# Performance work log

Measured on AMD Instinct MI355X. Metric: run time of the kernel, lower is better.

## Reference

```python
import jax, jax.numpy as jnp
import numpy as np

B, S, D = 2, 2048, 4096
N_HEADS, N_KV_HEADS, HEAD_DIM = 32, 8, 128
Q_DIM = N_HEADS * HEAD_DIM        # 4096
KV_DIM = N_KV_HEADS * HEAD_DIM    # 1024
N_REP = N_HEADS // N_KV_HEADS
ROPE_THETA = 500000.0


def make_freqs_cis(seqlen, head_dim, theta):
    # Interleaved (sin, cos) pairs per rotary frequency, matching the module's
    # einsum/flip RoPE convention: row1 = x0*sin + x1*cos, row0 = x0*cos - x1*sin.
    inv_freq = 1.0 / (theta ** (np.arange(0, head_dim, 2, dtype=np.float32) / head_dim))
    t = np.arange(seqlen, dtype=np.float32)
    ang = np.outer(t, inv_freq)                       # [S, hd/2]
    fc = np.stack([np.sin(ang), np.cos(ang)], axis=-1)  # [S, hd/2, 2]
    return jnp.asarray(fc.reshape(seqlen, head_dim))


def apply_rotary_emb(xq, xk, freqs_cis):
    # xq: [B,S,Hq,hd], xk: [B,S,Hkv,hd], freqs_cis: [S,hd]
    xq_shape, xk_shape = xq.shape, xk.shape
    xq2 = xq.reshape(*xq.shape[:-1], -1, 2)
    xk2 = xk.reshape(*xk.shape[:-1], -1, 2)
    fc = freqs_cis.reshape(freqs_cis.shape[0], 1, -1, 2)   # [S,1,hd/2,2]
    # row_1 = <x, fc>
    xq_row1 = jnp.einsum('bshpi,shpi->bshp', xq2, fc)
    xk_row1 = jnp.einsum('bshpi,shpi->bshp', xk2, fc)
    # flipped fc with negated second component: (f1, -f0)
    fc_flip = jnp.flip(fc, axis=-1) * jnp.array([1.0, -1.0], dtype=fc.dtype)
    xq_row0 = jnp.einsum('bshpi,shpi->bshp', xq2, fc_flip)
    xk_row0 = jnp.einsum('bshpi,shpi->bshp', xk2, fc_flip)
    xq_out = jnp.stack([xq_row0, xq_row1], axis=-1).reshape(xq_shape)
    xk_out = jnp.stack([xk_row0, xk_row1], axis=-1).reshape(xk_shape)
    return xq_out, xk_out


def setup_inputs() -> dict:
    key = jax.random.key(0)
    k1, k2, k3 = jax.random.split(key, 3)
    x = jax.random.normal(k1, (B, S, D), dtype=jnp.float32)
    wqkv = jax.random.normal(k2, (D, Q_DIM + 2 * KV_DIM), dtype=jnp.float32) * 0.02
    wo = jax.random.normal(k3, (Q_DIM, D), dtype=jnp.float32) * 0.02
    freqs_cis = make_freqs_cis(S, HEAD_DIM, ROPE_THETA)
    return {"x": x, "freqs_cis": freqs_cis, "wqkv": wqkv, "wo": wo, "is_causal": 1}


def reference(x, freqs_cis, wqkv, wo, is_causal):
    bsz, seqlen, _ = x.shape
    xqkv = jnp.einsum('bsd,de->bse', x, wqkv)
    xq = xqkv[..., :Q_DIM].reshape(bsz, seqlen, N_HEADS, HEAD_DIM)
    xk = xqkv[..., Q_DIM:Q_DIM + KV_DIM].reshape(bsz, seqlen, N_KV_HEADS, HEAD_DIM)
    xv = xqkv[..., Q_DIM + KV_DIM:].reshape(bsz, seqlen, N_KV_HEADS, HEAD_DIM)
    xq, xk = apply_rotary_emb(xq, xk, freqs_cis)
    # [B,H,S,hd]
    xq = xq.transpose(0, 2, 1, 3)
    xk = jnp.repeat(xk.transpose(0, 2, 1, 3), N_REP, axis=1)
    xv = jnp.repeat(xv.transpose(0, 2, 1, 3), N_REP, axis=1)
    scale = 1.0 / jnp.sqrt(jnp.asarray(HEAD_DIM, dtype=xq.dtype))
    scores = jnp.einsum('bhqd,bhkd->bhqk', xq, xk) * scale
    if is_causal:
        mask = jnp.tril(jnp.ones((seqlen, seqlen), dtype=bool))
        scores = jnp.where(mask, scores, jnp.finfo(scores.dtype).min)
    attn = jax.nn.softmax(scores, axis=-1)
    out = jnp.einsum('bhqk,bhkd->bhqd', attn, xv)
    out = out.transpose(0, 2, 1, 3).reshape(bsz, seqlen, Q_DIM)
    return jnp.einsum('bsd,de->bse', out, wo)
```

## Files before the change

### kernel.cpp

```cpp
#include <hip/hip_runtime.h>
#include <stdint.h>
#include <stddef.h>

#define BB 2
#define SS 2048
#define DD 4096
#define NH 32
#define NKV 8
#define HD 128
#define QDIM 4096
#define KVDIM 1024
#define NQKV 6144
#define NTILES 64
#define QK_SCALE_L2E 0.12751744f

typedef __bf16 bf16;
typedef __bf16 bf16x8 __attribute__((ext_vector_type(8)));
typedef __bf16 bf16x4 __attribute__((ext_vector_type(4)));
typedef float f32x4 __attribute__((ext_vector_type(4)));

#define MFMA16(a, b, c) __builtin_amdgcn_mfma_f32_16x16x32_bf16((a), (b), (c), 0, 0, 0)
#define BAR() __builtin_amdgcn_s_barrier()
#define VMW10() asm volatile("s_waitcnt vmcnt(10)" ::: "memory")
#define VMW8() asm volatile("s_waitcnt vmcnt(8)" ::: "memory")
#define VMW7() asm volatile("s_waitcnt vmcnt(7)" ::: "memory")

typedef __attribute__((address_space(1))) void GASV;
typedef __attribute__((address_space(3))) void LASV;

__device__ __forceinline__ void gload_lds16(const void* g, void* l) {
    __builtin_amdgcn_global_load_lds((GASV*)g, (LASV*)l, 16, 0, 0);
}

__device__ __forceinline__ float fexp2(float x) {
    float r;
    asm("v_exp_f32 %0, %1" : "=v"(r) : "v"(x));
    return r;
}

__global__ __launch_bounds__(256) void k_cvt_x(const float* __restrict__ in,
                                               bf16* __restrict__ out) {
    size_t i = ((size_t)blockIdx.x * 256 + threadIdx.x) * 8;
    const float4 a = *(const float4*)(in + i);
    const float4 b = *(const float4*)(in + i + 4);
    bf16x8 v;
    v[0] = (bf16)a.x; v[1] = (bf16)a.y; v[2] = (bf16)a.z; v[3] = (bf16)a.w;
    v[4] = (bf16)b.x; v[5] = (bf16)b.y; v[6] = (bf16)b.z; v[7] = (bf16)b.w;
    *(bf16x8*)(out + i) = v;
}

__global__ __launch_bounds__(256) void k_tr_cvt(const float* __restrict__ in,
                                                bf16* __restrict__ out, int R, int C) {
    __shared__ float tile[64][65];
    const int t = threadIdx.x;
    const int tx = t & 15, ty = t >> 4;
    const int r0 = blockIdx.y * 64, c0 = blockIdx.x * 64;
#pragma unroll
    for (int p = 0; p < 4; ++p) {
        const float4 v = *(const float4*)(in + (size_t)(r0 + p * 16 + ty) * C + c0 + tx * 4);
        tile[p * 16 + ty][tx * 4 + 0] = v.x;
        tile[p * 16 + ty][tx * 4 + 1] = v.y;
        tile[p * 16 + ty][tx * 4 + 2] = v.z;
        tile[p * 16 + ty][tx * 4 + 3] = v.w;
    }
    __syncthreads();
#pragma unroll
    for (int p = 0; p < 4; ++p) {
        const int oc = c0 + p * 16 + ty;
        bf16x4 pk;
#pragma unroll
        for (int j = 0; j < 4; ++j) pk[j] = (bf16)tile[tx * 4 + j][p * 16 + ty];
        *(bf16x4*)(out + (size_t)oc * R + r0 + tx * 4) = pk;
    }
}

__device__ __forceinline__ void stage_half(char* ldsRegion, const bf16* gsrc) {
    const int t = threadIdx.x;
    const int wid = t >> 6;
#pragma unroll
    for (int i = 0; i < 2; ++i) {
        const int off = i * 8192 + t * 16;
        const int row = off >> 7;
        const int pc = (off >> 4) & 7;
        const int lc = pc ^ (row & 7);
        gload_lds16(gsrc + (size_t)row * 4096 + lc * 8,
                    ldsRegion + i * 8192 + wid * 1024);
    }
}

__device__ __forceinline__ void gemm256(const bf16* __restrict__ At,
                                        const bf16* __restrict__ Bt,
                                        char* LB, f32x4 acc[8][4]) {
    const int tid = threadIdx.x, lane = tid & 63, wid = tid >> 6;
    const int wm = wid >> 2, wn = wid & 3;
    const int l15 = lane & 15, l4 = lane >> 4;

    const f32x4 vz = {0.f, 0.f, 0.f, 0.f};
#pragma unroll
    for (int m = 0; m < 8; ++m)
#pragma unroll
        for (int n = 0; n < 4; ++n) acc[m][n] = vz;

    auto Areg = [&](int db, int h) -> char* { return LB + db * 32768 + h * 16384; };
    auto Breg = [&](int db, int h) -> char* { return LB + 65536 + db * 32768 + h * 16384; };

    bf16x8 RA[2][4], RAb[2][4], RB0[2][2], RB1[2][2];

    auto loadA = [&](bf16x8 dst[2][4], int db, int h) {
        char* base = Areg(db, h);
#pragma unroll
        for (int kk = 0; kk < 2; ++kk)
#pragma unroll
            for (int mf = 0; mf < 4; ++mf) {
                const int row = wm * 64 + mf * 16 + l15;
                const int cc = kk * 4 + l4;
                dst[kk][mf] = *(const bf16x8*)(base + row * 128 + ((cc ^ (row & 7)) << 4));
            }
    };
    auto loadB = [&](bf16x8 dst[2][2], int db, int h) {
        char* base = Breg(db, h);
#pragma unroll
        for (int kk = 0; kk < 2; ++kk)
#pragma unroll
            for (int nf = 0; nf < 2; ++nf) {
                const int row = wn * 32 + nf * 16 + l15;
                const int cc = kk * 4 + l4;
                dst[kk][nf] = *(const bf16x8*)(base + row * 128 + ((cc ^ (row & 7)) << 4));
            }
    };
    auto stA = [&](int tau, int h) {
        stage_half(Areg(tau & 1, h), At + (size_t)(h * 128) * 4096 + tau * 64);
    };
    auto stB = [&](int tau, int h) {
        stage_half(Breg(tau & 1, h), Bt + (size_t)(h * 128) * 4096 + tau * 64);
    };
    auto mma = [&](bf16x8 A[2][4], bf16x8 B[2][2], int mb, int nb) {
        __builtin_amdgcn_s_setprio(1);
#pragma unroll
        for (int kk = 0; kk < 2; ++kk)
#pragma unroll
            for (int mf = 0; mf < 4; ++mf)
#pragma unroll
                for (int nf = 0; nf < 2; ++nf)
                    acc[mb + mf][nb + nf] = MFMA16(A[kk][mf], B[kk][nf], acc[mb + mf][nb + nf]);
        __builtin_amdgcn_s_setprio(0);
    };

    stA(0, 0); stB(0, 0); stB(0, 1); stA(0, 1);
    stA(1, 0); stB(1, 0); stB(1, 1); stA(1, 1);
    VMW8();
    BAR();
    loadA(RA, 0, 0); loadB(RB0, 0, 0);

#pragma unroll 1
    for (int tau = 0; tau < NTILES - 2; ++tau) {
        const int db = tau & 1, ndb = db ^ 1;
        loadB(RB1, db, 1);
        stA(tau + 2, 0);
        BAR();
        mma(RA, RB0, 0, 0);
        BAR();
        loadA(RAb, db, 1);
        stB(tau + 2, 0);
        BAR();
        mma(RA, RB1, 0, 2);
        BAR();
        stB(tau + 2, 1);
        VMW10();
        BAR();
        mma(RAb, RB0, 4, 0);
        BAR();
        loadA(RA, ndb, 0);
        loadB(RB0, ndb, 0);
        stA(tau + 2, 1);
        VMW8();
        BAR();
        mma(RAb, RB1, 4, 2);
        BAR();
    }

    asm volatile("s_waitcnt vmcnt(0)" ::: "memory");
    BAR();
#pragma unroll 1
    for (int tau = NTILES - 2; tau < NTILES; ++tau) {
        const int db = tau & 1, ndb = db ^ 1;
        loadB(RB1, db, 1);
        mma(RA, RB0, 0, 0);
        loadA(RAb, db, 1);
        mma(RA, RB1, 0, 2);
        mma(RAb, RB0, 4, 0);
        if (tau < NTILES - 1) { loadA(RA, ndb, 0); loadB(RB0, ndb, 0); }
        mma(RAb, RB1, 4, 2);
    }
}

__device__ __forceinline__ void stage_B192(char* ldsRegion, const bf16* gsrc) {
    const int t = threadIdx.x;
    const int wid = t >> 6;
#pragma unroll
    for (int i = 0; i < 3; ++i) {
        const int off = i * 8192 + t * 16;
        const int row = off >> 7;
        const int pc = (off >> 4) & 7;
        const int lc = pc ^ (row & 7);
        gload_lds16(gsrc + (size_t)row * 4096 + lc * 8,
                    ldsRegion + i * 8192 + wid * 1024);
    }
}

__device__ __forceinline__ void gemm192(const bf16* __restrict__ At,
                                        const bf16* __restrict__ Bt,
                                        char* LB, f32x4 acc[8][3]) {
    const int tid = threadIdx.x, lane = tid & 63, wid = tid >> 6;
    const int wm = wid >> 2, wn = wid & 3;
    const int l15 = lane & 15, l4 = lane >> 4;

    const f32x4 vz = {0.f, 0.f, 0.f, 0.f};
#pragma unroll
    for (int m = 0; m < 8; ++m)
#pragma unroll
        for (int n = 0; n < 3; ++n) acc[m][n] = vz;

    auto Areg = [&](int db, int h) -> char* { return LB + db * 32768 + h * 16384; };
    auto Breg = [&](int db) -> char* { return LB + 65536 + db * 24576; };

    bf16x8 RA[2][4], RAb[2][4], RB0[2][2], RB1[2];

    auto loadA = [&](bf16x8 dst[2][4], int db, int h) {
        char* base = Areg(db, h);
#pragma unroll
        for (int kk = 0; kk < 2; ++kk)
#pragma unroll
            for (int mf = 0; mf < 4; ++mf) {
                const int row = wm * 64 + mf * 16 + l15;
                const int cc = kk * 4 + l4;
                dst[kk][mf] = *(const bf16x8*)(base + row * 128 + ((cc ^ (row & 7)) << 4));
            }
    };
    auto loadB0 = [&](int db) {
        char* base = Breg(db);
#pragma unroll
        for (int kk = 0; kk < 2; ++kk)
#pragma unroll
            for (int nf = 0; nf < 2; ++nf) {
                const int row = wn * 48 + nf * 16 + l15;
                const int cc = kk * 4 + l4;
                RB0[kk][nf] = *(const bf16x8*)(base + row * 128 + ((cc ^ (row & 7)) << 4));
            }
    };
    auto loadB1 = [&](int db) {
        char* base = Breg(db);
#pragma unroll
        for (int kk = 0; kk < 2; ++kk) {
            const int row = wn * 48 + 32 + l15;
            const int cc = kk * 4 + l4;
            RB1[kk] = *(const bf16x8*)(base + row * 128 + ((cc ^ (row & 7)) << 4));
        }
    };
    auto stA = [&](int tau, int h) {
        stage_half(Areg(tau & 1, h), At + (size_t)(h * 128) * 4096 + tau * 64);
    };
    auto stB = [&](int tau) {
        stage_B192(Breg(tau & 1), Bt + tau * 64);
    };
    auto mmaB0 = [&](bf16x8 A[2][4], int mb) {
        __builtin_amdgcn_s_setprio(1);
#pragma unroll
        for (int kk = 0; kk < 2; ++kk)
#pragma unroll
            for (int mf = 0; mf < 4; ++mf)
#pragma unroll
                for (int nf = 0; nf < 2; ++nf)
                    acc[mb + mf][nf] = MFMA16(A[kk][mf], RB0[kk][nf], acc[mb + mf][nf]);
        __builtin_amdgcn_s_setprio(0);
    };
    auto mmaB1 = [&](bf16x8 A[2][4], int mb) {
        __builtin_amdgcn_s_setprio(1);
#pragma unroll
        for (int kk = 0; kk < 2; ++kk)
#pragma unroll
            for (int mf = 0; mf < 4; ++mf)
                acc[mb + mf][2] = MFMA16(A[kk][mf], RB1[kk], acc[mb + mf][2]);
        __builtin_amdgcn_s_setprio(0);
    };

    stA(0, 0); stB(0); stA(0, 1);
    stA(1, 0); stB(1); stA(1, 1);
    VMW7();
    BAR();
    loadA(RA, 0, 0); loadB0(0);

#pragma unroll 1
    for (int tau = 0; tau < NTILES - 2; ++tau) {
        const int db = tau & 1, ndb = db ^ 1;
        loadB1(db);
        stA(tau + 2, 0);
        BAR();
        mmaB0(RA, 0);
        BAR();
        loadA(RAb, db, 1);
        stB(tau + 2);
        BAR();
        mmaB1(RA, 0);
        BAR();
        stA(tau + 2, 1);
        VMW7();
        BAR();
        mmaB0(RAb, 4);
        BAR();
        loadA(RA, ndb, 0);
        loadB0(ndb);
        BAR();
        mmaB1(RAb, 4);
        BAR();
    }

    asm volatile("s_waitcnt vmcnt(0)" ::: "memory");
    BAR();
#pragma unroll 1
    for (int tau = NTILES - 2; tau < NTILES; ++tau) {
        const int db = tau & 1, ndb = db ^ 1;
        loadB1(db);
        mmaB0(RA, 0);
        loadA(RAb, db, 1);
        mmaB1(RA, 0);
        mmaB0(RAb, 4);
        if (tau < NTILES - 1) { loadA(RA, ndb, 0); loadB0(ndb); }
        mmaB1(RAb, 4);
    }
}

__device__ __forceinline__ void xcd_swizzle(int gx, int& bx, int& by) {
    const int nwg = gx * gridDim.y;
    int lin = by * gx + bx;
    lin = (lin & 7) * (nwg >> 3) + (lin >> 3);
    bx = lin % gx;
    by = lin / gx;
}

__global__ __launch_bounds__(512, 2) void k_gemm_qkv(const bf16* __restrict__ A,
                                                     const bf16* __restrict__ Bt,
                                                     const float* __restrict__ fc,
                                                     bf16* __restrict__ Qb,
                                                     bf16* __restrict__ Kb,
                                                     bf16* __restrict__ VTb) {
    __shared__ __align__(16) char LB[114688];
    f32x4 acc[8][3];
    int bx = blockIdx.x, by = blockIdx.y;
    xcd_swizzle(NQKV / 192, bx, by);
    gemm192(A + (size_t)by * 256 * 4096, Bt + (size_t)bx * 192 * 4096, LB, acc);

    const int tid = threadIdx.x, lane = tid & 63, wid = tid >> 6;
    const int wm = wid >> 2, wn = wid & 3;
    const int l15 = lane & 15, l4 = lane >> 4;
#pragma unroll
    for (int mf = 0; mf < 8; ++mf) {
        const int rowbase = by * 256 + (mf >> 2) * 128 + wm * 64 + (mf & 3) * 16 + l4 * 4;
#pragma unroll
        for (int nf = 0; nf < 3; ++nf) {
            const int rb = bx * 192 + wn * 48 + nf * 16;
            const int col = rb + l15;
            f32x4 v = acc[mf][nf];
            if (rb < QDIM + KVDIM) {
                const int d = col & (HD - 1);
                const int dp = d & ~1;
                const float sgn = (d & 1) ? 1.f : -1.f;
#pragma unroll
                for (int r = 0; r < 4; ++r) {
                    const int row = rowbase + r;
                    const int s = row & (SS - 1);
                    const float2 sc = *(const float2*)(fc + s * HD + dp);
                    const float partner = __shfl_xor(v[r], 1);
                    float res = v[r] * sc.y + sgn * partner * sc.x;
                    if (rb < QDIM) {
                        res *= QK_SCALE_L2E;
                        Qb[(size_t)row * QDIM + col] = (bf16)res;
                    } else {
                        Kb[(size_t)row * KVDIM + (col - QDIM)] = (bf16)res;
                    }
                }
            } else {
                const int hdv = col - (QDIM + KVDIM);
                const int kvh = hdv >> 7, dd = hdv & (HD - 1);
                const int bb = rowbase >> 11, s = rowbase & (SS - 1);
                bf16x4 pk;
#pragma unroll
                for (int r = 0; r < 4; ++r) pk[r] = (bf16)v[r];
                *(bf16x4*)(VTb + ((size_t)((bb * NKV + kvh) * HD + dd)) * SS + s) = pk;
            }
        }
    }
}

__global__ __launch_bounds__(512, 2) void k_gemm_out(const bf16* __restrict__ A,
                                                     const bf16* __restrict__ Bt,
                                                     float* __restrict__ out) {
    __shared__ __align__(16) char LB[131072];
    f32x4 acc[8][4];
    int bx = blockIdx.x, by = blockIdx.y;
    xcd_swizzle(DD / 256, bx, by);
    gemm256(A + (size_t)by * 256 * 4096, Bt + (size_t)bx * 256 * 4096, LB, acc);

    const int tid = threadIdx.x, lane = tid & 63, wid = tid >> 6;
    const int wm = wid >> 2, wn = wid & 3;
    const int l15 = lane & 15, l4 = lane >> 4;
#pragma unroll
    for (int mf = 0; mf < 8; ++mf) {
        const int row = by * 256 + (mf >> 2) * 128 + wm * 64 + (mf & 3) * 16 + l4 * 4;
#pragma unroll
        for (int nf = 0; nf < 4; ++nf) {
            const int col = bx * 256 + (nf >> 1) * 128 + wn * 32 + (nf & 1) * 16 + l15;
#pragma unroll
            for (int r = 0; r < 4; ++r) out[(size_t)(row + r) * DD + col] = acc[mf][nf][r];
        }
    }
}

__global__ __launch_bounds__(256, 2) void k_attn(const bf16* __restrict__ Qb,
                                                 const bf16* __restrict__ Kb,
                                                 const bf16* __restrict__ VTb,
                                                 bf16* __restrict__ Ob) {
    __shared__ __align__(16) bf16 Ks[64 * 128];
    __shared__ __align__(16) bf16 Vs[128 * 64];
    __shared__ __align__(16) bf16 Ps[4][32 * 88];
    int lin = (blockIdx.z * NH + blockIdx.y) * 8 + blockIdx.x;
    lin = (lin & 7) * 64 + (lin >> 3);
    const int jj = lin & 7, h = (lin >> 3) & (NH - 1), b = lin >> 8;
    const int kvh = h >> 2;
    const int tid = threadIdx.x, lane = tid & 63, w = tid >> 6;
    const int l15 = lane & 15, l4 = lane >> 4;

    const bf16* Kg = Kb + (size_t)b * SS * KVDIM + kvh * HD;
    const bf16* Vg = VTb + (size_t)(b * NKV + kvh) * HD * SS;

    int4 kreg[4], vreg[4];
    const f32x4 vz = {0.f, 0.f, 0.f, 0.f};

    auto issue_kv = [&](int t) {
#pragma unroll
        for (int i = 0; i < 4; ++i) {
            const int off = i * 4096 + tid * 16;
            const int row = off >> 8;
            const int cc = (off >> 4) & 15;
            kreg[i] = *(const int4*)((const char*)(Kg + (size_t)(t * 64 + row) * KVDIM) + cc * 16);
        }
#pragma unroll
        for (int i = 0; i < 4; ++i) {
            const int off = i * 4096 + tid * 16;
            const int row = off >> 7;
            const int cc = (off >> 4) & 7;
            vreg[i] = *(const int4*)((const char*)(Vg + (size_t)row * SS + t * 64) + cc * 16);
        }
    };

#pragma unroll 1
    for (int pj = 0; pj < 2; ++pj) {
        const int j = pj ? (15 - jj) : jj;
        const int q0 = j * 128;
        const int nt = 2 * j + 2;

        bf16x8 qf[2][4];
#pragma unroll
        for (int m = 0; m < 2; ++m) {
            const int qrow = q0 + w * 32 + m * 16 + l15;
            const bf16* qb = Qb + ((size_t)(b * SS + qrow) << 12) + h * HD + l4 * 8;
#pragma unroll
            for (int kc = 0; kc < 4; ++kc) qf[m][kc] = *(const bf16x8*)(qb + kc * 32);
        }

        f32x4 o[2][8];
#pragma unroll
        for (int m = 0; m < 2; ++m)
#pragma unroll
            for (int df = 0; df < 8; ++df) o[m][df] = vz;
        float m_run[2][4], l_run[2][4];
#pragma unroll
        for (int m = 0; m < 2; ++m)
#pragma unroll
            for (int r = 0; r < 4; ++r) { m_run[m][r] = -1e30f; l_run[m][r] = 0.f; }

        issue_kv(0);

        for (int t = 0; t < nt; ++t) {
            __syncthreads();
#pragma unroll
            for (int i = 0; i < 4; ++i) {
                const int off = i * 4096 + tid * 16;
                const int row = off >> 8;
                const int cc = (off >> 4) & 15;
                const int lc = cc ^ (row & 7);
                *(int4*)((char*)Ks + row * 256 + lc * 16) = kreg[i];
            }
#pragma unroll
            for (int i = 0; i < 4; ++i) {
                const int off = i * 4096 + tid * 16;
                const int row = off >> 7;
                const int cc = (off >> 4) & 7;
                const int lc = cc ^ (row & 7);
                *(int4*)((char*)Vs + row * 128 + lc * 16) = vreg[i];
            }
            __syncthreads();

            if (t + 1 < nt) issue_kv(t + 1);

            f32x4 sa[2][4];
#pragma unroll
            for (int m = 0; m < 2; ++m)
#pragma unroll
                for (int n = 0; n < 4; ++n) sa[m][n] = vz;
            __builtin_amdgcn_s_setprio(1);
#pragma unroll
            for (int kc = 0; kc < 4; ++kc)
#pragma unroll
                for (int n = 0; n < 4; ++n) {
                    const int krow = n * 16 + l15;
                    const int cc = kc * 4 + l4;
                    const bf16x8 kf =
                        *(const bf16x8*)((const char*)Ks + (krow << 8) + ((cc ^ (krow & 7)) << 4));
                    sa[0][n] = MFMA16(qf[0][kc], kf, sa[0][n]);
                    sa[1][n] = MFMA16(qf[1][kc], kf, sa[1][n]);
                }
            __builtin_amdgcn_s_setprio(0);

            if (t >= 2 * j) {
#pragma unroll
                for (int m = 0; m < 2; ++m)
#pragma unroll
                    for (int n = 0; n < 4; ++n)
#pragma unroll
                        for (int r = 0; r < 4; ++r) {
                            const int col = t * 64 + n * 16 + l15;
                            const int qr = q0 + w * 32 + m * 16 + l4 * 4 + r;
                            if (col > qr) sa[m][n][r] = -1e30f;
                        }
            }

#pragma unroll
            for (int m = 0; m < 2; ++m)
#pragma unroll
                for (int r = 0; r < 4; ++r) {
                    float mx = fmaxf(fmaxf(sa[m][0][r], sa[m][1][r]),
                                     fmaxf(sa[m][2][r], sa[m][3][r]));
#pragma unroll
                    for (int mk = 1; mk <= 8; mk <<= 1) mx = fmaxf(mx, __shfl_xor(mx, mk));
                    const float mn = fmaxf(m_run[m][r], mx);
                    const float alpha = fexp2(m_run[m][r] - mn);
                    m_run[m][r] = mn;
                    float rs = 0.f;
#pragma unroll
                    for (int n = 0; n < 4; ++n) {
                        const float p = fexp2(sa[m][n][r] - mn);
                        sa[m][n][r] = p;
                        rs += p;
                    }
#pragma unroll
                    for (int mk = 1; mk <= 8; mk <<= 1) rs += __shfl_xor(rs, mk);
                    l_run[m][r] = l_run[m][r] * alpha + rs;
#pragma unroll
                    for (int df = 0; df < 8; ++df) o[m][df][r] *= alpha;
                }

#pragma unroll
            for (int m = 0; m < 2; ++m)
#pragma unroll
                for (int n = 0; n < 4; ++n)
#pragma unroll
                    for (int r = 0; r < 4; ++r)
                        Ps[w][(m * 16 + l4 * 4 + r) * 88 + n * 16 + l15] = (bf16)sa[m][n][r];

            bf16x8 pf0[2], pf1[2];
#pragma unroll
            for (int ks = 0; ks < 2; ++ks) {
                pf0[ks] = *(const bf16x8*)(&Ps[w][l15 * 88 + ks * 32 + l4 * 8]);
                pf1[ks] = *(const bf16x8*)(&Ps[w][(16 + l15) * 88 + ks * 32 + l4 * 8]);
            }

            __builtin_amdgcn_s_setprio(1);
#pragma unroll
            for (int df = 0; df < 8; ++df)
#pragma unroll
                for (int ks = 0; ks < 2; ++ks) {
                    const int vrow = df * 16 + l15;
                    const int cc = ks * 4 + l4;
                    const bf16x8 vf =
                        *(const bf16x8*)((const char*)Vs + (vrow << 7) + ((cc ^ (vrow & 7)) << 4));
                    o[0][df] = MFMA16(pf0[ks], vf, o[0][df]);
                    o[1][df] = MFMA16(pf1[ks], vf, o[1][df]);
                }
            __builtin_amdgcn_s_setprio(0);
        }

#pragma unroll
        for (int m = 0; m < 2; ++m)
#pragma unroll
            for (int r = 0; r < 4; ++r) {
                const float inv = 1.f / l_run[m][r];
                const size_t row = (size_t)(b * SS + q0 + w * 32 + m * 16 + l4 * 4 + r);
#pragma unroll
                for (int df = 0; df < 8; ++df)
                    Ob[(row << 12) + h * HD + df * 16 + l15] = (bf16)(o[m][df][r] * inv);
            }
    }
}

extern "C" void kernel_launch(void* const* d_in, const int* in_sizes, int n_in,
                              void* d_out, int out_size, void* d_ws, size_t ws_size,
                              hipStream_t stream) {
    const float* x    = (const float*)d_in[0];
    const float* fc   = (const float*)d_in[1];
    const float* wqkv = (const float*)d_in[2];
    const float* wo   = (const float*)d_in[3];

    char* wsp = (char*)d_ws;
    const size_t MB = (size_t)1 << 20;
    bf16* xb    = (bf16*)(wsp);
    bf16* wqkvT = (bf16*)(wsp + 32 * MB);
    bf16* woT   = (bf16*)(wsp + 32 * MB);
    bf16* Qb    = (bf16*)(wsp + 80 * MB);
    bf16* Kb    = (bf16*)(wsp + 112 * MB);
    bf16* VTb   = (bf16*)(wsp + 120 * MB);
    bf16* Ab    = (bf16*)(wsp);
    float* out  = (float*)d_out;

    k_cvt_x<<<8192, 256, 0, stream>>>(x, xb);
    k_tr_cvt<<<dim3(NQKV / 64, DD / 64), 256, 0, stream>>>(wqkv, wqkvT, DD, NQKV);
    k_gemm_qkv<<<dim3(NQKV / 192, (BB * SS) / 256), 512, 0, stream>>>(xb, wqkvT, fc, Qb, Kb, VTb);
    k_tr_cvt<<<dim3(DD / 64, QDIM / 64), 256, 0, stream>>>(wo, woT, QDIM, DD);
    k_attn<<<dim3(8, NH, BB), 256, 0, stream>>>(Qb, Kb, VTb, Ab);
    k_gemm_out<<<dim3(DD / 256, (BB * SS) / 256), 512, 0, stream>>>(Ab, woT, out);
}
```

Measured before the change: 571.1 us.

## Restructure GEMM mainloops to single-tile prefetch with explicit sched barriers

Both GEMM mainloops drop from a two-tile-ahead prefetch with register-level cross-iteration LDS reads to a one-tile-ahead prefetch. LDS fragments are now read at the start of each iteration, with explicit lgkmcnt waits and sched_barrier fences to pin the instruction order. The vmcnt thresholds and the epilogue change to match. The aim is a simpler, more predictable interleave of global-to-LDS staging and MFMA, at the cost of less latency hiding for global loads. Merging the last two MFMA phases also removes one barrier per iteration.

New measurement: 569.5 us. Within noise of the previous version (-0.3%).

```diff
diff --git a/kernel.cpp b/kernel.cpp
--- a/kernel.cpp
+++ b/kernel.cpp
@@ -20,10 +20,20 @@
 typedef float f32x4 __attribute__((ext_vector_type(4)));
 
 #define MFMA16(a, b, c) __builtin_amdgcn_mfma_f32_16x16x32_bf16((a), (b), (c), 0, 0, 0)
-#define BAR() __builtin_amdgcn_s_barrier()
-#define VMW10() asm volatile("s_waitcnt vmcnt(10)" ::: "memory")
-#define VMW8() asm volatile("s_waitcnt vmcnt(8)" ::: "memory")
-#define VMW7() asm volatile("s_waitcnt vmcnt(7)" ::: "memory")
+#define VMW5() asm volatile("s_waitcnt vmcnt(5)" ::: "memory")
+#define VMW4() asm volatile("s_waitcnt vmcnt(4)" ::: "memory")
+#define VMW2() asm volatile("s_waitcnt vmcnt(2)" ::: "memory")
+#define VMW0() asm volatile("s_waitcnt vmcnt(0)" ::: "memory")
+#define BARX()                                  \
+    do {                                        \
+        __builtin_amdgcn_s_barrier();           \
+        __builtin_amdgcn_sched_barrier(0);      \
+    } while (0)
+#define LGKM0_SGB()                                         \
+    do {                                                    \
+        asm volatile("s_waitcnt lgkmcnt(0)" ::: "memory");  \
+        __builtin_amdgcn_sched_barrier(0);                  \
+    } while (0)
 
 typedef __attribute__((address_space(1))) void GASV;
 typedef __attribute__((address_space(3))) void LASV;
@@ -146,50 +156,47 @@
         __builtin_amdgcn_s_setprio(0);
     };
 
-    stA(0, 0); stB(0, 0); stB(0, 1); stA(0, 1);
-    stA(1, 0); stB(1, 0); stB(1, 1); stA(1, 1);
-    VMW8();
-    BAR();
-    loadA(RA, 0, 0); loadB(RB0, 0, 0);
+    stA(0, 0); stB(0, 0);
+    stB(0, 1); stA(0, 1);
+    VMW4();
+    BARX();
 
 #pragma unroll 1
-    for (int tau = 0; tau < NTILES - 2; ++tau) {
-        const int db = tau & 1, ndb = db ^ 1;
+    for (int tau = 0; tau < NTILES - 1; ++tau) {
+        const int db = tau & 1;
+        loadA(RA, db, 0);
+        loadB(RB0, db, 0);
+        stA(tau + 1, 0);
+        stB(tau + 1, 0);
+        VMW4();
+        BARX(); LGKM0_SGB();
+        mma(RA, RB0, 0, 0);
+        BARX();
         loadB(RB1, db, 1);
-        stA(tau + 2, 0);
-        BAR();
+        stB(tau + 1, 1);
+        stA(tau + 1, 1);
+        BARX(); LGKM0_SGB();
+        mma(RA, RB1, 0, 2);
+        BARX();
+        loadA(RAb, db, 1);
+        VMW4();
+        BARX(); LGKM0_SGB();
+        mma(RAb, RB0, 4, 0);
+        mma(RAb, RB1, 4, 2);
+        BARX();
+    }
+
+    VMW0();
+    BARX();
+    {
+        const int db = (NTILES - 1) & 1;
+        loadA(RA, db, 0);
+        loadB(RB0, db, 0);
         mma(RA, RB0, 0, 0);
-        BAR();
+        loadB(RB1, db, 1);
+        mma(RA, RB1, 0, 2);
         loadA(RAb, db, 1);
-        stB(tau + 2, 0);
-        BAR();
-        mma(RA, RB1, 0, 2);
-        BAR();
-        stB(tau + 2, 1);
-        VMW10();
-        BAR();
         mma(RAb, RB0, 4, 0);
-        BAR();
-        loadA(RA, ndb, 0);
-        loadB(RB0, ndb, 0);
-        stA(tau + 2, 1);
-        VMW8();
-        BAR();
-        mma(RAb, RB1, 4, 2);
-        BAR();
-    }
-
-    asm volatile("s_waitcnt vmcnt(0)" ::: "memory");
-    BAR();
-#pragma unroll 1
-    for (int tau = NTILES - 2; tau < NTILES; ++tau) {
-        const int db = tau & 1, ndb = db ^ 1;
-        loadB(RB1, db, 1);
-        mma(RA, RB0, 0, 0);
-        loadA(RAb, db, 1);
-        mma(RA, RB1, 0, 2);
-        mma(RAb, RB0, 4, 0);
-        if (tau < NTILES - 1) { loadA(RA, ndb, 0); loadB(RB0, ndb, 0); }
         mma(RAb, RB1, 4, 2);
     }
 }
@@ -284,48 +291,46 @@
         __builtin_amdgcn_s_setprio(0);
     };
 
-    stA(0, 0); stB(0); stA(0, 1);
-    stA(1, 0); stB(1); stA(1, 1);
-    VMW7();
-    BAR();
-    loadA(RA, 0, 0); loadB0(0);
+    stA(0, 0); stB(0);
+    stA(0, 1);
+    VMW2();
+    BARX();
 
 #pragma unroll 1
-    for (int tau = 0; tau < NTILES - 2; ++tau) {
-        const int db = tau & 1, ndb = db ^ 1;
+    for (int tau = 0; tau < NTILES - 1; ++tau) {
+        const int db = tau & 1;
+        loadA(RA, db, 0);
+        loadB0(db);
+        stA(tau + 1, 0);
+        stB(tau + 1);
+        VMW5();
+        BARX(); LGKM0_SGB();
+        mmaB0(RA, 0);
+        BARX();
         loadB1(db);
-        stA(tau + 2, 0);
-        BAR();
+        stA(tau + 1, 1);
+        BARX(); LGKM0_SGB();
+        mmaB1(RA, 0);
+        BARX();
+        loadA(RAb, db, 1);
+        VMW2();
+        BARX(); LGKM0_SGB();
+        mmaB0(RAb, 4);
+        mmaB1(RAb, 4);
+        BARX();
+    }
+
+    VMW0();
+    BARX();
+    {
+        const int db = (NTILES - 1) & 1;
+        loadA(RA, db, 0);
+        loadB0(db);
         mmaB0(RA, 0);
-        BAR();
+        loadB1(db);
+        mmaB1(RA, 0);
         loadA(RAb, db, 1);
-        stB(tau + 2);
-        BAR();
-        mmaB1(RA, 0);
-        BAR();
-        stA(tau + 2, 1);
-        VMW7();
-        BAR();
         mmaB0(RAb, 4);
-        BAR();
-        loadA(RA, ndb, 0);
-        loadB0(ndb);
-        BAR();
-        mmaB1(RAb, 4);
-        BAR();
-    }
-
-    asm volatile("s_waitcnt vmcnt(0)" ::: "memory");
-    BAR();
-#pragma unroll 1
-    for (int tau = NTILES - 2; tau < NTILES; ++tau) {
-        const int db = tau & 1, ndb = db ^ 1;
-        loadB1(db);
-        mmaB0(RA, 0);
-        loadA(RAb, db, 1);
-        mmaB1(RA, 0);
-        mmaB0(RAb, 4);
-        if (tau < NTILES - 1) { loadA(RA, ndb, 0); loadB0(ndb); }
         mmaB1(RAb, 4);
     }
 }
```
